# Performance work log

Hardware: AMD Instinct MI355X
Metric: run time of the kernel (lower is better)

The kernel has to match this reference:

```python
import jax, jax.numpy as jnp
import numpy as np

E, HID, T, B, NH, DFF, A, C = 116, 64, 512, 64, 4, 2048, 116, 90


def _ln(x, g, b, eps=1e-5):
    m = x.mean(-1, keepdims=True)
    v = ((x - m) ** 2).mean(-1, keepdims=True)
    return (x - m) / jnp.sqrt(v + eps) * g + b


def _layer(x, p):
    # torch TransformerEncoderLayer, post-norm, relu, eval mode (no dropout)
    wqkv, bqkv, wo, bo, g1, bn1, w1, b1, w2, b2, g2, bn2 = p
    S, N, Em = x.shape  # note: S is the attended axis (dim 0), N the batched axis
    dh = Em // NH
    qkv = x @ wqkv.T + bqkv
    q, k, v = jnp.split(qkv, 3, axis=-1)
    q = q.reshape(S, N, NH, dh)
    k = k.reshape(S, N, NH, dh)
    v = v.reshape(S, N, NH, dh)
    scores = jnp.einsum('snhd,tnhd->nhst', q, k) / np.float32(np.sqrt(dh))
    attn = jax.nn.softmax(scores, axis=-1)
    o = jnp.einsum('nhst,tnhd->snhd', attn, v).reshape(S, N, Em)
    o = o @ wo.T + bo
    x = _ln(x + o, g1, bn1)
    f = jax.nn.relu(x @ w1.T + b1) @ w2.T + b2
    return _ln(x + f, g2, bn2)


def _forward(x, sim, p1, p2, fc_w, fc_b):
    out = _layer(x, p1)
    out1 = _layer(out, p2)
    outs = jnp.transpose(out1, (0, 2, 1))       # (B, E, T)
    fea_ = outs @ fc_w.T + fc_b                 # (B, E, HID)
    feas = jnp.transpose(fea_, (0, 2, 1))       # (B, HID, E)
    fea = feas[:, None, :, :, None]             # (B,1,HID,E,1)
    sim32 = sim.astype(jnp.float32)             # (A, HID, C)
    # cosine_similarity over the HID axis (dim=2 of broadcast tensors),
    # computed without materializing the (B,A,HID,E,C) broadcast product.
    dot = jnp.einsum('bhd,ahc->badc', feas, sim32)           # (B,A,E,C)
    fn = jnp.linalg.norm(feas, axis=1)                       # (B,E)
    sn = jnp.linalg.norm(sim32, axis=1)                      # (A,C)
    denom = jnp.maximum(fn[:, None, :, None] * sn[None, :, None, :], 1e-8)
    similarity = dot / denom                                 # (B,A,E,C)
    similar = similarity.reshape(-1, 116 * 90)
    nrm = jnp.maximum(jnp.linalg.norm(similar, axis=1, keepdims=True), 1e-12)
    similar = similar / nrm
    return fea, similarity, similar


_PNAMES = ['wqkv', 'bqkv', 'wo', 'bo', 'g1', 'bn1', 'w1', 'b1', 'w2', 'b2', 'g2', 'bn2']
_PSHAPES = [(3 * E, E), (3 * E,), (E, E), (E,), (E,), (E,), (DFF, E), (DFF,), (E, DFF), (E,), (E,), (E,)]


def setup_inputs() -> dict:
    key = jax.random.key(0)
    ks = jax.random.split(key, 32)
    s = 0.02
    inp = {
        'x': jax.random.normal(ks[0], (B, T, E), jnp.float32),
        'sim': jax.random.normal(ks[1], (A, HID, C), jnp.float32),
    }
    i = 2
    for L in ('l1', 'l2'):
        for nm, sh in zip(_PNAMES, _PSHAPES):
            if nm in ('g1', 'g2'):
                inp[f'{L}_{nm}'] = jnp.ones(sh, jnp.float32)
            elif nm in ('bqkv', 'bo', 'bn1', 'b1', 'b2', 'bn2'):
                inp[f'{L}_{nm}'] = jnp.zeros(sh, jnp.float32)
            else:
                inp[f'{L}_{nm}'] = jax.random.normal(ks[i], sh, jnp.float32) * s
                i += 1
    inp['fc_w'] = jax.random.normal(ks[i], (HID, T), jnp.float32) * s
    inp['fc_b'] = jnp.zeros((HID,), jnp.float32)
    return inp


def reference(x, sim,
              l1_wqkv, l1_bqkv, l1_wo, l1_bo, l1_g1, l1_bn1, l1_w1, l1_b1, l1_w2, l1_b2, l1_g2, l1_bn2,
              l2_wqkv, l2_bqkv, l2_wo, l2_bo, l2_g1, l2_bn1, l2_w1, l2_b1, l2_w2, l2_b2, l2_g2, l2_bn2,
              fc_w, fc_b):
    p1 = (l1_wqkv, l1_bqkv, l1_wo, l1_bo, l1_g1, l1_bn1, l1_w1, l1_b1, l1_w2, l1_b2, l1_g2, l1_bn2)
    p2 = (l2_wqkv, l2_bqkv, l2_wo, l2_bo, l2_g1, l2_bn1, l2_w1, l2_b1, l2_w2, l2_b2, l2_g2, l2_bn2)
    return _forward(x, sim, p1, p2, fc_w, fc_b)
```

## Files before the change

kernel.cpp:

```cpp
#include <hip/hip_runtime.h>
#include <hip/hip_bf16.h>

typedef __attribute__((ext_vector_type(8))) short short8v;
typedef __attribute__((ext_vector_type(4))) float floatx4;

__device__ __forceinline__ float bf2f(unsigned short u) {
  union { unsigned int i; float f; } c;
  c.i = ((unsigned int)u) << 16;
  return c.f;
}
__device__ __forceinline__ unsigned short f2bf(float f) {
  __hip_bfloat16 h = __float2bfloat16(f);
  return *reinterpret_cast<unsigned short*>(&h);
}

struct ConvJobs {
  const float* src[9];
  unsigned short* dst[9];
  int K[9];
  int Kp[9];
  int mode[9];
  int cum[10];
};

__global__ __launch_bounds__(256) void convert_all_kernel(ConvJobs J) {
  const int total = J.cum[9];
  for (int idx = blockIdx.x * 256 + threadIdx.x; idx < total;
       idx += gridDim.x * 256) {
    int j = 0;
    while (idx >= J.cum[j + 1]) ++j;
    const int local = idx - J.cum[j];
    const int Kp = J.Kp[j];
    const int r = local / Kp, c = local - r * Kp;
    unsigned short v;
    if (J.mode[j] == 0) {
      v = (c < J.K[j]) ? f2bf(J.src[j][(size_t)r * J.K[j] + c])
                       : (unsigned short)0;
    } else {
      const int h = c >> 5, d = c & 31;
      v = (d < 29) ? f2bf(J.src[j][(size_t)r * 116 + h * 29 + d])
                   : (unsigned short)0;
    }
    J.dst[j][local] = v;
  }
}

template <int MODE>
__global__ __launch_bounds__(256) void mgemm_kernel(
    const unsigned short* __restrict__ A, const unsigned short* __restrict__ B,
    const float* __restrict__ bias, int N, int Kp, int ldout,
    unsigned short* __restrict__ Yb) {
  __shared__ __align__(16) unsigned short As[128][64];
  __shared__ __align__(16) unsigned short Bs[128][64];

  const int tid = threadIdx.x;
  const int M0 = blockIdx.x * 128;
  const int N0 = blockIdx.y * 128;
  const int wid = tid >> 6, lane = tid & 63;
  const int wr = wid >> 1, wc = wid & 1;
  const int lc = lane & 15, g = lane >> 4;
  const int srow = tid >> 1, shalf = tid & 1;
  const int sw = srow & 7;

  floatx4 acc[4][4] = {};

  const int nk = Kp >> 6;
  for (int kt = 0; kt < nk; ++kt) {
    const int k0 = kt << 6;
    {
      const uint4* p = reinterpret_cast<const uint4*>(
          A + (size_t)(M0 + srow) * Kp + k0 + shalf * 32);
      uint4 v0 = p[0], v1 = p[1], v2 = p[2], v3 = p[3];
      *reinterpret_cast<uint4*>(&As[srow][((((shalf << 2) | 0) ^ sw) << 3)]) = v0;
      *reinterpret_cast<uint4*>(&As[srow][((((shalf << 2) | 1) ^ sw) << 3)]) = v1;
      *reinterpret_cast<uint4*>(&As[srow][((((shalf << 2) | 2) ^ sw) << 3)]) = v2;
      *reinterpret_cast<uint4*>(&As[srow][((((shalf << 2) | 3) ^ sw) << 3)]) = v3;
    }
    {
      uint4 v0 = {0, 0, 0, 0}, v1 = v0, v2 = v0, v3 = v0;
      const int jr = N0 + srow;
      if (jr < N) {
        const uint4* p = reinterpret_cast<const uint4*>(
            B + (size_t)jr * Kp + k0 + shalf * 32);
        v0 = p[0]; v1 = p[1]; v2 = p[2]; v3 = p[3];
      }
      *reinterpret_cast<uint4*>(&Bs[srow][((((shalf << 2) | 0) ^ sw) << 3)]) = v0;
      *reinterpret_cast<uint4*>(&Bs[srow][((((shalf << 2) | 1) ^ sw) << 3)]) = v1;
      *reinterpret_cast<uint4*>(&Bs[srow][((((shalf << 2) | 2) ^ sw) << 3)]) = v2;
      *reinterpret_cast<uint4*>(&Bs[srow][((((shalf << 2) | 3) ^ sw) << 3)]) = v3;
    }
    __syncthreads();
#pragma unroll
    for (int ks = 0; ks < 2; ++ks) {
      short8v a[4], b[4];
#pragma unroll
      for (int m = 0; m < 4; ++m) {
        const int row = wr * 64 + m * 16 + lc;
        a[m] = *reinterpret_cast<const short8v*>(
            &As[row][((((ks << 2) | g) ^ (lc & 7)) << 3)]);
      }
#pragma unroll
      for (int n = 0; n < 4; ++n) {
        const int col = wc * 64 + n * 16 + lc;
        b[n] = *reinterpret_cast<const short8v*>(
            &Bs[col][((((ks << 2) | g) ^ (lc & 7)) << 3)]);
      }
#pragma unroll
      for (int m = 0; m < 4; ++m)
#pragma unroll
        for (int n = 0; n < 4; ++n)
          acc[m][n] = __builtin_amdgcn_mfma_f32_16x16x32_bf16(a[m], b[n],
                                                              acc[m][n], 0, 0, 0);
    }
    __syncthreads();
  }

#pragma unroll
  for (int m = 0; m < 4; ++m) {
#pragma unroll
    for (int r = 0; r < 4; ++r) {
      const int row = M0 + wr * 64 + m * 16 + g * 4 + r;
#pragma unroll
      for (int n = 0; n < 4; ++n) {
        const int col = N0 + wc * 64 + n * 16 + lc;
        if (col < N) {
          float v = acc[m][n][r] + bias[col];
          if (MODE == 1) v = fmaxf(v, 0.f);
          if constexpr (MODE == 3) {
            const int which = (col >= 232) ? 2 : (col >= 116 ? 1 : 0);
            const int cw = col - which * 116;
            const int h = (cw * 565) >> 14;
            const int d = cw - h * 29;
            const int nn2 = row & 511, ss = row >> 9;
            Yb[(size_t)which * 4194304 +
               ((((size_t)nn2 * 4 + h) * 64 + ss) << 5) + d] = f2bf(v);
          } else {
            Yb[(size_t)row * ldout + col] = f2bf(v);
          }
        }
      }
    }
  }
}

__global__ __launch_bounds__(256) void mgemm64_ln_kernel(
    const unsigned short* __restrict__ A, const unsigned short* __restrict__ B,
    const float* __restrict__ bias, int Kp, unsigned short* __restrict__ Yb,
    float* __restrict__ Yf, const float* __restrict__ res,
    const float* __restrict__ gw, const float* __restrict__ bw) {
  __shared__ __align__(16) unsigned short As[64][64];
  __shared__ __align__(16) unsigned short Bs[128][64];
  __shared__ float sum1[2][64];
  __shared__ float sum2[2][64];

  const int tid = threadIdx.x;
  const int M0 = blockIdx.x * 64;
  const int wid = tid >> 6, lane = tid & 63;
  const int wr = wid >> 1, wc = wid & 1;
  const int lc = lane & 15, g = lane >> 4;
  const int arow = tid >> 2, aq = tid & 3;
  const int brow = tid >> 1, bhalf = tid & 1;

  floatx4 acc[2][4] = {};

  const int nk = Kp >> 6;
  for (int kt = 0; kt < nk; ++kt) {
    const int k0 = kt << 6;
    {
      const uint4* p = reinterpret_cast<const uint4*>(
          A + (size_t)(M0 + arow) * Kp + k0 + aq * 16);
      uint4 v0 = p[0], v1 = p[1];
      const int swa = arow & 7;
      *reinterpret_cast<uint4*>(&As[arow][(((aq * 2) ^ swa) << 3)]) = v0;
      *reinterpret_cast<uint4*>(&As[arow][(((aq * 2 + 1) ^ swa) << 3)]) = v1;
    }
    {
      uint4 v0 = {0, 0, 0, 0}, v1 = v0, v2 = v0, v3 = v0;
      if (brow < 116) {
        const uint4* p = reinterpret_cast<const uint4*>(
            B + (size_t)brow * Kp + k0 + bhalf * 32);
        v0 = p[0]; v1 = p[1]; v2 = p[2]; v3 = p[3];
      }
      const int sw = brow & 7;
      *reinterpret_cast<uint4*>(&Bs[brow][((((bhalf << 2) | 0) ^ sw) << 3)]) = v0;
      *reinterpret_cast<uint4*>(&Bs[brow][((((bhalf << 2) | 1) ^ sw) << 3)]) = v1;
      *reinterpret_cast<uint4*>(&Bs[brow][((((bhalf << 2) | 2) ^ sw) << 3)]) = v2;
      *reinterpret_cast<uint4*>(&Bs[brow][((((bhalf << 2) | 3) ^ sw) << 3)]) = v3;
    }
    __syncthreads();
#pragma unroll
    for (int ks = 0; ks < 2; ++ks) {
      short8v a[2], b[4];
#pragma unroll
      for (int m = 0; m < 2; ++m) {
        const int row = wr * 32 + m * 16 + lc;
        a[m] = *reinterpret_cast<const short8v*>(
            &As[row][((((ks << 2) | g) ^ (row & 7)) << 3)]);
      }
#pragma unroll
      for (int n = 0; n < 4; ++n) {
        const int col = wc * 64 + n * 16 + lc;
        b[n] = *reinterpret_cast<const short8v*>(
            &Bs[col][((((ks << 2) | g) ^ (col & 7)) << 3)]);
      }
#pragma unroll
      for (int m = 0; m < 2; ++m)
#pragma unroll
        for (int n = 0; n < 4; ++n)
          acc[m][n] = __builtin_amdgcn_mfma_f32_16x16x32_bf16(a[m], b[n],
                                                              acc[m][n], 0, 0, 0);
    }
    __syncthreads();
  }

  float s1l[2][4], s2l[2][4];
#pragma unroll
  for (int m = 0; m < 2; ++m) {
#pragma unroll
    for (int r = 0; r < 4; ++r) {
      const int row = M0 + wr * 32 + m * 16 + g * 4 + r;
      float s = 0.f, s2 = 0.f;
#pragma unroll
      for (int n = 0; n < 4; ++n) {
        const int col = wc * 64 + n * 16 + lc;
        float v = 0.f;
        if (col < 116)
          v = acc[m][n][r] + bias[col] + res[(size_t)row * 116 + col];
        acc[m][n][r] = v;
        s += v;
        s2 = fmaf(v, v, s2);
      }
#pragma unroll
      for (int st = 1; st < 16; st <<= 1) {
        s += __shfl_xor(s, st, 16);
        s2 += __shfl_xor(s2, st, 16);
      }
      s1l[m][r] = s;
      s2l[m][r] = s2;
    }
  }
  if (lc == 0) {
#pragma unroll
    for (int m = 0; m < 2; ++m)
#pragma unroll
      for (int r = 0; r < 4; ++r) {
        const int lrow = wr * 32 + m * 16 + g * 4 + r;
        sum1[wc][lrow] = s1l[m][r];
        sum2[wc][lrow] = s2l[m][r];
      }
  }
  __syncthreads();
#pragma unroll
  for (int m = 0; m < 2; ++m) {
#pragma unroll
    for (int r = 0; r < 4; ++r) {
      const int lrow = wr * 32 + m * 16 + g * 4 + r;
      const int row = M0 + lrow;
      const float st = sum1[0][lrow] + sum1[1][lrow];
      const float s2t = sum2[0][lrow] + sum2[1][lrow];
      const float mean = st * (1.f / 116.f);
      const float var = s2t * (1.f / 116.f) - mean * mean;
      const float rstd = 1.f / sqrtf(var + 1e-5f);
#pragma unroll
      for (int n = 0; n < 4; ++n) {
        const int col = wc * 64 + n * 16 + lc;
        if (col < 116) {
          const float y = (acc[m][n][r] - mean) * rstd * gw[col] + bw[col];
          Yf[(size_t)row * 116 + col] = y;
          Yb[(size_t)row * 128 + col] = f2bf(y);
        } else {
          Yb[(size_t)row * 128 + col] = 0;
        }
      }
    }
  }
}

__global__ __launch_bounds__(256) void ffn_fused_kernel(
    const unsigned short* __restrict__ Xa,
    const unsigned short* __restrict__ W1,
    const float* __restrict__ b1,
    const unsigned short* __restrict__ W2,
    const float* __restrict__ b2, const float* __restrict__ res,
    const float* __restrict__ gw, const float* __restrict__ bw,
    unsigned short* __restrict__ Yb,
    float* __restrict__ Yf) {
  __shared__ __align__(16) unsigned short Xs[64][128];
  __shared__ __align__(16) unsigned short W1c[64][128];
  __shared__ __align__(16) unsigned short W2c[128][64];
  __shared__ __align__(16) unsigned short Hs[64][64];
  __shared__ float sum1[2][64];
  __shared__ float sum2[2][64];

  const int tid = threadIdx.x;
  const int M0 = blockIdx.x * 64;
  const int wid = tid >> 6, lane = tid & 63;
  const int wr = wid >> 1, wc = wid & 1;
  const int lc = lane & 15, g = lane >> 4;
  const int arow = tid >> 2, aq = tid & 3;
  const int brow = tid >> 1, bh = tid & 1;

  {
    const uint4* p = reinterpret_cast<const uint4*>(
        Xa + (size_t)(M0 + arow) * 128 + aq * 32);
#pragma unroll
    for (int q = 0; q < 4; ++q) {
      const int cj = aq * 4 + q;
      const int swz = (cj & 8) | ((cj ^ arow) & 7);
      *reinterpret_cast<uint4*>(&Xs[arow][swz * 8]) = p[q];
    }
  }

  uint4 w1r[4], w2r[4];
  {
    const uint4* p1 =
        reinterpret_cast<const uint4*>(W1 + (size_t)arow * 128 + aq * 32);
#pragma unroll
    for (int q = 0; q < 4; ++q) w1r[q] = p1[q];
    uint4 z = {0, 0, 0, 0};
    w2r[0] = z; w2r[1] = z; w2r[2] = z; w2r[3] = z;
    if (brow < 116) {
      const uint4* p2 =
          reinterpret_cast<const uint4*>(W2 + (size_t)brow * 2048 + bh * 32);
#pragma unroll
      for (int q = 0; q < 4; ++q) w2r[q] = p2[q];
    }
  }

  floatx4 oacc[2][4] = {};

  for (int kc = 0; kc < 32; ++kc) {
#pragma unroll
    for (int q = 0; q < 4; ++q) {
      const int cj = aq * 4 + q;
      const int swz = (cj & 8) | ((cj ^ arow) & 7);
      *reinterpret_cast<uint4*>(&W1c[arow][swz * 8]) = w1r[q];
    }
#pragma unroll
    for (int q = 0; q < 4; ++q) {
      const int cj = bh * 4 + q;
      const int swz = (cj ^ brow) & 7;
      *reinterpret_cast<uint4*>(&W2c[brow][swz * 8]) = w2r[q];
    }
    if (kc < 31) {
      const uint4* p1 = reinterpret_cast<const uint4*>(
          W1 + (size_t)((kc + 1) * 64 + arow) * 128 + aq * 32);
#pragma unroll
      for (int q = 0; q < 4; ++q) w1r[q] = p1[q];
      if (brow < 116) {
        const uint4* p2 = reinterpret_cast<const uint4*>(
            W2 + (size_t)brow * 2048 + (kc + 1) * 64 + bh * 32);
#pragma unroll
        for (int q = 0; q < 4; ++q) w2r[q] = p2[q];
      }
    }
    __syncthreads();

    floatx4 hacc[2][2] = {};
#pragma unroll
    for (int ks = 0; ks < 4; ++ks) {
      short8v av[2], bv[2];
#pragma unroll
      for (int m = 0; m < 2; ++m) {
        const int row = wr * 32 + m * 16 + lc;
        const int cj = ks * 4 + g;
        const int swz = (cj & 8) | ((cj ^ row) & 7);
        av[m] = *reinterpret_cast<const short8v*>(&Xs[row][swz * 8]);
      }
#pragma unroll
      for (int n = 0; n < 2; ++n) {
        const int row = wc * 32 + n * 16 + lc;
        const int cj = ks * 4 + g;
        const int swz = (cj & 8) | ((cj ^ row) & 7);
        bv[n] = *reinterpret_cast<const short8v*>(&W1c[row][swz * 8]);
      }
#pragma unroll
      for (int m = 0; m < 2; ++m)
#pragma unroll
        for (int n = 0; n < 2; ++n)
          hacc[m][n] = __builtin_amdgcn_mfma_f32_16x16x32_bf16(av[m], bv[n],
                                                               hacc[m][n], 0, 0, 0);
    }
#pragma unroll
    for (int n = 0; n < 2; ++n) {
      const int dff = wc * 32 + n * 16 + lc;
      const float bb = b1[kc * 64 + dff];
      const int cj = dff >> 3;
      const int dlo = dff & 7;
#pragma unroll
      for (int m = 0; m < 2; ++m) {
#pragma unroll
        for (int r = 0; r < 4; ++r) {
          const int tok = wr * 32 + m * 16 + g * 4 + r;
          const float hv = fmaxf(hacc[m][n][r] + bb, 0.f);
          Hs[tok][(((cj ^ tok) & 7) << 3) | dlo] = f2bf(hv);
        }
      }
    }
    __syncthreads();

#pragma unroll
    for (int ks = 0; ks < 2; ++ks) {
      short8v av[2], bv[4];
#pragma unroll
      for (int m = 0; m < 2; ++m) {
        const int row = wr * 32 + m * 16 + lc;
        const int cj = ks * 4 + g;
        av[m] = *reinterpret_cast<const short8v*>(
            &Hs[row][(((cj ^ row) & 7) << 3)]);
      }
#pragma unroll
      for (int n = 0; n < 4; ++n) {
        const int col = wc * 64 + n * 16 + lc;
        const int cj = ks * 4 + g;
        bv[n] = *reinterpret_cast<const short8v*>(
            &W2c[col][(((cj ^ col) & 7) << 3)]);
      }
#pragma unroll
      for (int m = 0; m < 2; ++m)
#pragma unroll
        for (int n = 0; n < 4; ++n)
          oacc[m][n] = __builtin_amdgcn_mfma_f32_16x16x32_bf16(av[m], bv[n],
                                                               oacc[m][n], 0, 0, 0);
    }
    __syncthreads();
  }

  float s1l[2][4], s2l[2][4];
#pragma unroll
  for (int m = 0; m < 2; ++m) {
#pragma unroll
    for (int r = 0; r < 4; ++r) {
      const int row = M0 + wr * 32 + m * 16 + g * 4 + r;
      float s = 0.f, s2 = 0.f;
#pragma unroll
      for (int n = 0; n < 4; ++n) {
        const int col = wc * 64 + n * 16 + lc;
        float v = 0.f;
        if (col < 116)
          v = oacc[m][n][r] + b2[col] + res[(size_t)row * 116 + col];
        oacc[m][n][r] = v;
        s += v;
        s2 = fmaf(v, v, s2);
      }
#pragma unroll
      for (int st = 1; st < 16; st <<= 1) {
        s += __shfl_xor(s, st, 16);
        s2 += __shfl_xor(s2, st, 16);
      }
      s1l[m][r] = s;
      s2l[m][r] = s2;
    }
  }
  if (lc == 0) {
#pragma unroll
    for (int m = 0; m < 2; ++m)
#pragma unroll
      for (int r = 0; r < 4; ++r) {
        const int lrow = wr * 32 + m * 16 + g * 4 + r;
        sum1[wc][lrow] = s1l[m][r];
        sum2[wc][lrow] = s2l[m][r];
      }
  }
  __syncthreads();
#pragma unroll
  for (int m = 0; m < 2; ++m) {
#pragma unroll
    for (int r = 0; r < 4; ++r) {
      const int lrow = wr * 32 + m * 16 + g * 4 + r;
      const int row = M0 + lrow;
      const float st = sum1[0][lrow] + sum1[1][lrow];
      const float s2t = sum2[0][lrow] + sum2[1][lrow];
      const float mean = st * (1.f / 116.f);
      const float var = s2t * (1.f / 116.f) - mean * mean;
      const float rstd = 1.f / sqrtf(var + 1e-5f);
#pragma unroll
      for (int n = 0; n < 4; ++n) {
        const int col = wc * 64 + n * 16 + lc;
        if (col < 116) {
          const float y = (oacc[m][n][r] - mean) * rstd * gw[col] + bw[col];
          Yf[(size_t)row * 116 + col] = y;
          Yb[(size_t)row * 128 + col] = f2bf(y);
        } else {
          Yb[(size_t)row * 128 + col] = 0;
        }
      }
    }
  }
}

__global__ __launch_bounds__(64) void attn_kernel(
    const unsigned short* __restrict__ qkvp, unsigned short* __restrict__ obuf) {
  const int h = blockIdx.x & 3;
  const int n = blockIdx.x >> 2;
  const int s = threadIdx.x;
  __shared__ float ks[64][36];
  __shared__ float vs[64][36];

  const size_t rb = (((size_t)n * 4 + h) * 64 + s) * 32;
  const uint4* qp = reinterpret_cast<const uint4*>(qkvp + rb);
  const uint4* kp = reinterpret_cast<const uint4*>(qkvp + 4194304 + rb);
  const uint4* vp = reinterpret_cast<const uint4*>(qkvp + 8388608 + rb);
  uint4 qv[4], kv4[4], vv4[4];
#pragma unroll
  for (int i = 0; i < 4; ++i) {
    qv[i] = qp[i];
    kv4[i] = kp[i];
    vv4[i] = vp[i];
  }
  float q[32], kf[32], vf[32];
#pragma unroll
  for (int i = 0; i < 4; ++i) {
    const unsigned* wq = reinterpret_cast<const unsigned*>(&qv[i]);
    const unsigned* wk = reinterpret_cast<const unsigned*>(&kv4[i]);
    const unsigned* wv = reinterpret_cast<const unsigned*>(&vv4[i]);
#pragma unroll
    for (int j = 0; j < 4; ++j) {
      union { unsigned u; float f; } lo, hi;
      const int d0 = i * 8 + 2 * j;
      lo.u = wq[j] << 16; hi.u = wq[j] & 0xffff0000u;
      q[d0] = lo.f; q[d0 + 1] = hi.f;
      lo.u = wk[j] << 16; hi.u = wk[j] & 0xffff0000u;
      kf[d0] = (d0 < 29) ? lo.f : 0.f;
      kf[d0 + 1] = (d0 + 1 < 29) ? hi.f : 0.f;
      lo.u = wv[j] << 16; hi.u = wv[j] & 0xffff0000u;
      vf[d0] = (d0 < 29) ? lo.f : 0.f;
      vf[d0 + 1] = (d0 + 1 < 29) ? hi.f : 0.f;
    }
  }
  q[29] = q[30] = q[31] = 0.f;
#pragma unroll
  for (int c = 0; c < 8; ++c) {
    *reinterpret_cast<float4*>(&ks[s][c * 4]) =
        make_float4(kf[4 * c], kf[4 * c + 1], kf[4 * c + 2], kf[4 * c + 3]);
    *reinterpret_cast<float4*>(&vs[s][c * 4]) =
        make_float4(vf[4 * c], vf[4 * c + 1], vf[4 * c + 2], vf[4 * c + 3]);
  }
  __syncthreads();

  const float scale = 0.18569533817705186f;
  float sc[64];
#pragma unroll 4
  for (int t = 0; t < 64; ++t) {
    const float4* kr = reinterpret_cast<const float4*>(&ks[t][0]);
    float a = 0.f;
#pragma unroll
    for (int c = 0; c < 8; ++c) {
      const float4 kc = kr[c];
      a = fmaf(q[4 * c], kc.x, a);
      a = fmaf(q[4 * c + 1], kc.y, a);
      a = fmaf(q[4 * c + 2], kc.z, a);
      a = fmaf(q[4 * c + 3], kc.w, a);
    }
    sc[t] = a * scale;
  }
  float m = sc[0];
#pragma unroll
  for (int t = 1; t < 64; ++t) m = fmaxf(m, sc[t]);
  float sum = 0.f;
#pragma unroll
  for (int t = 0; t < 64; ++t) {
    sc[t] = __expf(sc[t] - m);
    sum += sc[t];
  }
  const float inv = 1.f / sum;
  float o[32] = {};
#pragma unroll 4
  for (int t = 0; t < 64; ++t) {
    const float p = sc[t];
    const float4* vr = reinterpret_cast<const float4*>(&vs[t][0]);
#pragma unroll
    for (int c = 0; c < 8; ++c) {
      const float4 vc = vr[c];
      o[4 * c] = fmaf(p, vc.x, o[4 * c]);
      o[4 * c + 1] = fmaf(p, vc.y, o[4 * c + 1]);
      o[4 * c + 2] = fmaf(p, vc.z, o[4 * c + 2]);
      o[4 * c + 3] = fmaf(p, vc.w, o[4 * c + 3]);
    }
  }
  unsigned short ow[32];
#pragma unroll
  for (int i = 0; i < 32; ++i) ow[i] = f2bf(o[i] * inv);
  uint4* od =
      reinterpret_cast<uint4*>(obuf + ((size_t)s * 512 + n) * 128 + h * 32);
  const uint4* ows = reinterpret_cast<const uint4*>(ow);
#pragma unroll
  for (int i = 0; i < 4; ++i) od[i] = ows[i];
}

__global__ __launch_bounds__(256) void fc_kernel(
    const float* __restrict__ X4, const float* __restrict__ fw,
    const float* __restrict__ fb, float* __restrict__ fea,
    unsigned short* __restrict__ feaT, float* __restrict__ fn) {
  const int eg = blockIdx.x;
  const int b = blockIdx.y;
  const int e0 = eg * 29;
  __shared__ float Os[64][30];
  __shared__ float Wf[64][65];
  const int tid = threadIdx.x;
  const int h = tid & 63, jg = tid >> 6;
  float acc[8] = {};

  for (int tc = 0; tc < 8; ++tc) {
    for (int idx = tid; idx < 64 * 29; idx += 256) {
      int tt = idx / 29;
      int ee = idx - tt * 29;
      Os[tt][ee] = X4[((size_t)b * 512 + tc * 64 + tt) * 116 + e0 + ee];
    }
    for (int idx = tid; idx < 64 * 64; idx += 256) {
      int hh = idx >> 6, t2 = idx & 63;
      Wf[hh][t2] = fw[(size_t)hh * 512 + tc * 64 + t2];
    }
    __syncthreads();
#pragma unroll 4
    for (int t = 0; t < 64; ++t) {
      const float w = Wf[h][t];
#pragma unroll
      for (int m = 0; m < 8; ++m) {
        const int el = jg + 4 * m;
        if (el < 29) acc[m] = fmaf(Os[t][el], w, acc[m]);
      }
    }
    __syncthreads();
  }
  const float bb = fb[h];
#pragma unroll
  for (int m = 0; m < 8; ++m) {
    const int el = jg + 4 * m;
    if (el < 29) {
      const float v = acc[m] + bb;
      const int e = e0 + el;
      fea[((size_t)b * 64 + h) * 116 + e] = v;
      if (feaT) {
        const unsigned short vb = f2bf(v);
        feaT[((size_t)b * 128 + e) * 64 + h] = vb;
        float s = bf2f(vb);
        s = s * s;
#pragma unroll
        for (int st = 1; st <= 32; st <<= 1) s += __shfl_xor(s, st, 64);
        if (h == 0) fn[b * 128 + e] = sqrtf(s);
      }
    }
  }
}

__global__ __launch_bounds__(256) void simt_prep_kernel(
    const float* __restrict__ simin, unsigned short* __restrict__ simT,
    float* __restrict__ sn) {
  __shared__ float L[64][91];
  const int a = blockIdx.x;
  const int tid = threadIdx.x;
  for (int idx = tid; idx < 64 * 90; idx += 256) {
    const int h = idx / 90, c = idx - h * 90;
    L[h][c] = bf2f(f2bf(simin[((size_t)a * 64 + h) * 90 + c]));
  }
  __syncthreads();
  for (int idx = tid; idx < 96 * 64; idx += 256) {
    const int c = idx >> 6, h = idx & 63;
    simT[((size_t)a * 96 + c) * 64 + h] = (c < 90) ? f2bf(L[h][c]) : 0;
  }
  if (tid < 90) {
    float s = 0.f;
#pragma unroll 8
    for (int h = 0; h < 64; ++h) {
      const float t = L[h][tid];
      s = fmaf(t, t, s);
    }
    sn[a * 96 + tid] = sqrtf(s);
  }
}

__global__ __launch_bounds__(256) void sim_mfma3_kernel(
    const unsigned short* __restrict__ feaT, const unsigned short* __restrict__ simT,
    const float* __restrict__ fn, const float* __restrict__ sn,
    float* __restrict__ simil, float* __restrict__ similar) {
  const int a0 = blockIdx.x * 4;
  const int b = blockIdx.y;
  __shared__ __align__(16) unsigned short Ft[128][64];
  __shared__ __align__(16) unsigned short St[96][64];
  __shared__ __align__(16) float Rs[10440];
  __shared__ float fnrow[116];
  __shared__ float snrow[90];
  __shared__ float wred[4];
  const int tid = threadIdx.x;
  const int srow = tid >> 1, shalf = tid & 1;
  const int sw = srow & 7;
  const int wid = tid >> 6, lane = tid & 63;
  const int wr = wid >> 1, wc = wid & 1;
  const int lc = lane & 15, g = lane >> 4;

  {
    const uint4* p = reinterpret_cast<const uint4*>(
        feaT + ((size_t)b * 128 + srow) * 64 + shalf * 32);
    uint4 v0 = p[0], v1 = p[1], v2 = p[2], v3 = p[3];
    *reinterpret_cast<uint4*>(&Ft[srow][((((shalf << 2) | 0) ^ sw) << 3)]) = v0;
    *reinterpret_cast<uint4*>(&Ft[srow][((((shalf << 2) | 1) ^ sw) << 3)]) = v1;
    *reinterpret_cast<uint4*>(&Ft[srow][((((shalf << 2) | 2) ^ sw) << 3)]) = v2;
    *reinterpret_cast<uint4*>(&Ft[srow][((((shalf << 2) | 3) ^ sw) << 3)]) = v3;
  }
  if (tid < 116) fnrow[tid] = fn[b * 128 + tid];

  for (int ai = 0; ai < 4; ++ai) {
    const int a = a0 + ai;
    if (srow < 96) {
      const uint4* p = reinterpret_cast<const uint4*>(
          simT + ((size_t)a * 96 + srow) * 64 + shalf * 32);
      uint4 v0 = p[0], v1 = p[1], v2 = p[2], v3 = p[3];
      *reinterpret_cast<uint4*>(&St[srow][((((shalf << 2) | 0) ^ sw) << 3)]) = v0;
      *reinterpret_cast<uint4*>(&St[srow][((((shalf << 2) | 1) ^ sw) << 3)]) = v1;
      *reinterpret_cast<uint4*>(&St[srow][((((shalf << 2) | 2) ^ sw) << 3)]) = v2;
      *reinterpret_cast<uint4*>(&St[srow][((((shalf << 2) | 3) ^ sw) << 3)]) = v3;
    }
    if (tid >= 160 && tid < 250) snrow[tid - 160] = sn[a * 96 + (tid - 160)];
    __syncthreads();

    floatx4 acc[4][3] = {};
#pragma unroll
    for (int ks = 0; ks < 2; ++ks) {
      short8v av[4], bv[3];
#pragma unroll
      for (int m = 0; m < 4; ++m) {
        const int row = wr * 64 + m * 16 + lc;
        av[m] = *reinterpret_cast<const short8v*>(
            &Ft[row][((((ks << 2) | g) ^ (lc & 7)) << 3)]);
      }
#pragma unroll
      for (int n = 0; n < 3; ++n) {
        const int col = wc * 48 + n * 16 + lc;
        bv[n] = *reinterpret_cast<const short8v*>(
            &St[col][((((ks << 2) | g) ^ (lc & 7)) << 3)]);
      }
#pragma unroll
      for (int m = 0; m < 4; ++m)
#pragma unroll
        for (int n = 0; n < 3; ++n)
          acc[m][n] = __builtin_amdgcn_mfma_f32_16x16x32_bf16(av[m], bv[n],
                                                              acc[m][n], 0, 0, 0);
    }

    float ss = 0.f;
#pragma unroll
    for (int m = 0; m < 4; ++m) {
#pragma unroll
      for (int r = 0; r < 4; ++r) {
        const int d = wr * 64 + m * 16 + g * 4 + r;
        if (d < 116) {
          const float fnv = fnrow[d];
#pragma unroll
          for (int n = 0; n < 3; ++n) {
            const int c = wc * 48 + n * 16 + lc;
            if (c < 90) {
              const float denom = fmaxf(fnv * snrow[c], 1e-8f);
              float rcp = __builtin_amdgcn_rcpf(denom);
              rcp = rcp * (2.0f - denom * rcp);
              const float v = acc[m][n][r] * rcp;
              ss = fmaf(v, v, ss);
              Rs[d * 90 + c] = v;
            }
          }
        }
      }
    }
#pragma unroll
    for (int st = 1; st <= 32; st <<= 1) ss += __shfl_xor(ss, st, 64);
    if (lane == 0) wred[wid] = ss;
    __syncthreads();
    const float tot = wred[0] + wred[1] + wred[2] + wred[3];
    const float inv = 1.f / fmaxf(sqrtf(tot), 1e-12f);

    const size_t rowbase = ((size_t)b * 116 + a) * (116 * 90);
    float4* so = reinterpret_cast<float4*>(simil + rowbase);
    float4* sr = reinterpret_cast<float4*>(similar + rowbase);
    const float4* rs4 = reinterpret_cast<const float4*>(Rs);
    for (int i = tid; i < 2610; i += 256) {
      float4 v = rs4[i];
      so[i] = v;
      float4 w;
      w.x = v.x * inv; w.y = v.y * inv; w.z = v.z * inv; w.w = v.w * inv;
      sr[i] = w;
    }
  }
}

__global__ __launch_bounds__(256) void sim_mfma_kernel(
    const float* __restrict__ fea, const float* __restrict__ simin,
    float* __restrict__ simil, float* __restrict__ similar) {
  const int a = blockIdx.x;
  const int b = blockIdx.y;
  __shared__ __align__(16) unsigned char shmem[41760];
  __shared__ float fnrow[116];
  __shared__ float snrow[90];
  __shared__ float wred[4];
  const int tid = threadIdx.x;

  unsigned short (*Ft)[64] = reinterpret_cast<unsigned short(*)[64]>(shmem);
  unsigned short (*St)[64] =
      reinterpret_cast<unsigned short(*)[64]>(shmem + 16384);
  float* Rs = reinterpret_cast<float*>(shmem);

  for (int idx = tid; idx < 64 * 116; idx += 256) {
    const int h = idx / 116, d = idx - h * 116;
    Ft[d][(((h >> 3) ^ (d & 7)) << 3) | (h & 7)] =
        f2bf(fea[((size_t)b * 64 + h) * 116 + d]);
  }
  for (int idx = tid; idx < 12 * 64; idx += 256) {
    const int d = 116 + (idx >> 6), h = idx & 63;
    Ft[d][(((h >> 3) ^ (d & 7)) << 3) | (h & 7)] = 0;
  }
  for (int idx = tid; idx < 64 * 90; idx += 256) {
    const int h = idx / 90, c = idx - h * 90;
    St[c][(((h >> 3) ^ (c & 7)) << 3) | (h & 7)] =
        f2bf(simin[((size_t)a * 64 + h) * 90 + c]);
  }
  for (int idx = tid; idx < 6 * 64; idx += 256) {
    const int c = 90 + (idx >> 6), h = idx & 63;
    St[c][(((h >> 3) ^ (c & 7)) << 3) | (h & 7)] = 0;
  }
  __syncthreads();

  if (tid < 116) {
    float s = 0.f;
#pragma unroll 8
    for (int h = 0; h < 64; ++h) {
      const float t = bf2f(Ft[tid][(((h >> 3) ^ (tid & 7)) << 3) | (h & 7)]);
      s = fmaf(t, t, s);
    }
    fnrow[tid] = sqrtf(s);
  } else if (tid >= 128 && tid < 218) {
    const int c = tid - 128;
    float s = 0.f;
#pragma unroll 8
    for (int h = 0; h < 64; ++h) {
      const float t = bf2f(St[c][(((h >> 3) ^ (c & 7)) << 3) | (h & 7)]);
      s = fmaf(t, t, s);
    }
    snrow[c] = sqrtf(s);
  }
  __syncthreads();

  const int wid = tid >> 6, lane = tid & 63;
  const int wr = wid >> 1, wc = wid & 1;
  const int lc = lane & 15, g = lane >> 4;

  floatx4 acc[4][3] = {};
#pragma unroll
  for (int ks = 0; ks < 2; ++ks) {
    short8v av[4], bv[3];
#pragma unroll
    for (int m = 0; m < 4; ++m) {
      const int row = wr * 64 + m * 16 + lc;
      av[m] = *reinterpret_cast<const short8v*>(
          &Ft[row][((((ks << 2) | g) ^ (lc & 7)) << 3)]);
    }
#pragma unroll
    for (int n = 0; n < 3; ++n) {
      const int col = wc * 48 + n * 16 + lc;
      bv[n] = *reinterpret_cast<const short8v*>(
          &St[col][((((ks << 2) | g) ^ (lc & 7)) << 3)]);
    }
#pragma unroll
    for (int m = 0; m < 4; ++m)
#pragma unroll
      for (int n = 0; n < 3; ++n)
        acc[m][n] = __builtin_amdgcn_mfma_f32_16x16x32_bf16(av[m], bv[n],
                                                            acc[m][n], 0, 0, 0);
  }
  __syncthreads();

  float ss = 0.f;
#pragma unroll
  for (int m = 0; m < 4; ++m) {
#pragma unroll
    for (int r = 0; r < 4; ++r) {
      const int d = wr * 64 + m * 16 + g * 4 + r;
      if (d < 116) {
        const float fnv = fnrow[d];
#pragma unroll
        for (int n = 0; n < 3; ++n) {
          const int c = wc * 48 + n * 16 + lc;
          if (c < 90) {
            const float denom = fmaxf(fnv * snrow[c], 1e-8f);
            float rcp = __builtin_amdgcn_rcpf(denom);
            rcp = rcp * (2.0f - denom * rcp);
            const float v = acc[m][n][r] * rcp;
            ss = fmaf(v, v, ss);
            Rs[d * 90 + c] = v;
          }
        }
      }
    }
  }
#pragma unroll
  for (int st = 1; st <= 32; st <<= 1) ss += __shfl_xor(ss, st, 64);
  if (lane == 0) wred[wid] = ss;
  __syncthreads();
  const float tot = wred[0] + wred[1] + wred[2] + wred[3];
  const float inv = 1.f / fmaxf(sqrtf(tot), 1e-12f);

  const size_t rowbase = ((size_t)b * 116 + a) * (116 * 90);
  float4* so = reinterpret_cast<float4*>(simil + rowbase);
  float4* sr = reinterpret_cast<float4*>(similar + rowbase);
  const float4* rs4 = reinterpret_cast<const float4*>(Rs);
  for (int i = tid; i < 2610; i += 256) {
    float4 v = rs4[i];
    so[i] = v;
    float4 w;
    w.x = v.x * inv; w.y = v.y * inv; w.z = v.z * inv; w.w = v.w * inv;
    sr[i] = w;
  }
}

extern "C" void kernel_launch(void* const* d_in, const int* in_sizes, int n_in,
                              void* d_out, int out_size, void* d_ws,
                              size_t ws_size, hipStream_t stream) {
  const float* x0 = (const float*)d_in[0];
  const float* simin = (const float*)d_in[1];
  const float* p[24];
  for (int i = 0; i < 24; ++i) p[i] = (const float*)d_in[2 + i];
  const float* fc_w = (const float*)d_in[26];
  const float* fc_b = (const float*)d_in[27];

  float* out = (float*)d_out;
  float* fea = out;
  float* simil = out + 475136;
  float* similar = out + 77981696;

  float* xa_f[2] = {similar + 0, similar + 7602176};
  float* xb_f[2] = {similar + 3801088, similar + 11403264};
  unsigned short* obufb = (unsigned short*)(similar + 15204352);
  unsigned short* qkvp = (unsigned short*)(similar + 17301504);
  unsigned short* Ab = (unsigned short*)(similar + 23592960);
  unsigned short* xab[2] = {(unsigned short*)(similar + 25690112),
                            (unsigned short*)(similar + 29884416)};
  unsigned short* xbb[2] = {(unsigned short*)(similar + 27787264),
                            (unsigned short*)(similar + 31981568)};
  unsigned short* wbuf = (unsigned short*)(simil + 33554432);
  const size_t WSZ = 559104;

  unsigned char* ws = (unsigned char*)d_ws;
  unsigned short* feaT = (unsigned short*)ws;
  unsigned short* simT = (unsigned short*)(ws + 1048576);
  float* fnb = (float*)(ws + 2473984);
  float* snb = (float*)(ws + 2506752);
  const bool ws_ok = ws_size >= 2551296;

  {
    ConvJobs J;
    int cum = 0;
    auto add = [&](int j, const float* s, unsigned short* dd, int R, int K,
                   int Kp, int mode) {
      J.src[j] = s; J.dst[j] = dd; J.K[j] = K; J.Kp[j] = Kp; J.mode[j] = mode;
      J.cum[j] = cum; cum += R * Kp;
    };
    add(0, x0, Ab, 32768, 116, 128, 0);
    for (int L = 0; L < 2; ++L) {
      unsigned short* wb = wbuf + L * WSZ;
      add(1 + L * 4, p[L * 12 + 0], wb + 0, 348, 116, 128, 0);
      add(2 + L * 4, p[L * 12 + 2], wb + 44544, 116, 116, 128, 1);
      add(3 + L * 4, p[L * 12 + 6], wb + 59392, 2048, 116, 128, 0);
      add(4 + L * 4, p[L * 12 + 8], wb + 321536, 116, 2048, 2048, 0);
    }
    J.cum[9] = cum;
    hipLaunchKernelGGL(convert_all_kernel, dim3(2048), dim3(256), 0, stream, J);
  }

  if (ws_ok) {
    hipLaunchKernelGGL(simt_prep_kernel, dim3(116), dim3(256), 0, stream,
                       simin, simT, snb);
  }

  const unsigned short* Ain = Ab;
  const float* resin = x0;
  for (int L = 0; L < 2; ++L) {
    unsigned short* wb = wbuf + L * WSZ;
    const float* bqkv = p[L * 12 + 1];
    const float* bo = p[L * 12 + 3];
    const float* g1 = p[L * 12 + 4];
    const float* bn1 = p[L * 12 + 5];
    const float* b1 = p[L * 12 + 7];
    const float* b2 = p[L * 12 + 9];
    const float* g2 = p[L * 12 + 10];
    const float* bn2 = p[L * 12 + 11];

    hipLaunchKernelGGL((mgemm_kernel<3>), dim3(256, 3), dim3(256), 0, stream,
                       Ain, wb + 0, bqkv, 348, 128, 0, qkvp);
    hipLaunchKernelGGL(attn_kernel, dim3(2048), dim3(64), 0, stream, qkvp,
                       obufb);
    hipLaunchKernelGGL(mgemm64_ln_kernel, dim3(512), dim3(256), 0, stream,
                       obufb, wb + 44544, bo, 128, xab[L], xa_f[L], resin, g1,
                       bn1);
    hipLaunchKernelGGL(ffn_fused_kernel, dim3(512), dim3(256), 0, stream,
                       xab[L], wb + 59392, b1, wb + 321536, b2, xa_f[L], g2,
                       bn2, xbb[L], xb_f[L]);
    Ain = xbb[L];
    resin = xb_f[L];
  }

  if (ws_ok) {
    hipLaunchKernelGGL(fc_kernel, dim3(4, 64), dim3(256), 0, stream, xb_f[1],
                       fc_w, fc_b, fea, feaT, fnb);
    hipLaunchKernelGGL(sim_mfma3_kernel, dim3(29, 64), dim3(256), 0, stream,
                       feaT, simT, fnb, snb, simil, similar);
  } else {
    hipLaunchKernelGGL(fc_kernel, dim3(4, 64), dim3(256), 0, stream, xb_f[1],
                       fc_w, fc_b, fea, (unsigned short*)nullptr,
                       (float*)nullptr);
    hipLaunchKernelGGL(sim_mfma_kernel, dim3(116, 64), dim3(256), 0, stream,
                       fea, simin, simil, similar);
  }
}
```

Measured before the change: 664.5 us.

## Warp-specialize similarity kernel to overlap MFMA compute with output stores

The similarity kernel now runs 512 threads split into two roles. The first 256 compute the MFMA tile for one anchor and prefetch the next anchor's sim tile into a double buffer. The second 256 normalize and write the previous anchor's results to global memory. This is meant to hide the large store traffic (two float outputs of about 41 KB per anchor) behind compute, in exchange for roughly double the LDS footprint and lower occupancy (launch_bounds 512,1).

After: 675.1 us. Within noise of the previous version (+1.6%).

```diff
diff --git a/kernel.cpp b/kernel.cpp
--- a/kernel.cpp
+++ b/kernel.cpp
@@ -277,14 +277,11 @@
 }
 
 __global__ __launch_bounds__(256) void ffn_fused_kernel(
-    const unsigned short* __restrict__ Xa,
-    const unsigned short* __restrict__ W1,
-    const float* __restrict__ b1,
-    const unsigned short* __restrict__ W2,
+    const unsigned short* __restrict__ Xa, const unsigned short* __restrict__ W1,
+    const float* __restrict__ b1, const unsigned short* __restrict__ W2,
     const float* __restrict__ b2, const float* __restrict__ res,
     const float* __restrict__ gw, const float* __restrict__ bw,
-    unsigned short* __restrict__ Yb,
-    float* __restrict__ Yf) {
+    unsigned short* __restrict__ Yb, float* __restrict__ Yf) {
   __shared__ __align__(16) unsigned short Xs[64][128];
   __shared__ __align__(16) unsigned short W1c[64][128];
   __shared__ __align__(16) unsigned short W2c[128][64];
@@ -670,115 +667,136 @@
   }
 }
 
-__global__ __launch_bounds__(256) void sim_mfma3_kernel(
+__global__ __launch_bounds__(512, 1) void sim_mfma4_kernel(
     const unsigned short* __restrict__ feaT, const unsigned short* __restrict__ simT,
     const float* __restrict__ fn, const float* __restrict__ sn,
     float* __restrict__ simil, float* __restrict__ similar) {
   const int a0 = blockIdx.x * 4;
   const int b = blockIdx.y;
   __shared__ __align__(16) unsigned short Ft[128][64];
-  __shared__ __align__(16) unsigned short St[96][64];
-  __shared__ __align__(16) float Rs[10440];
+  __shared__ __align__(16) unsigned short St[2][96][64];
+  __shared__ __align__(16) float Rs[2][10440];
   __shared__ float fnrow[116];
-  __shared__ float snrow[90];
-  __shared__ float wred[4];
+  __shared__ float snrow[2][90];
+  __shared__ float wred[2][4];
   const int tid = threadIdx.x;
-  const int srow = tid >> 1, shalf = tid & 1;
-  const int sw = srow & 7;
   const int wid = tid >> 6, lane = tid & 63;
-  const int wr = wid >> 1, wc = wid & 1;
-  const int lc = lane & 15, g = lane >> 4;
 
   {
+    const int row = tid >> 2, q4 = tid & 3;
+    const int sw = row & 7;
     const uint4* p = reinterpret_cast<const uint4*>(
-        feaT + ((size_t)b * 128 + srow) * 64 + shalf * 32);
-    uint4 v0 = p[0], v1 = p[1], v2 = p[2], v3 = p[3];
-    *reinterpret_cast<uint4*>(&Ft[srow][((((shalf << 2) | 0) ^ sw) << 3)]) = v0;
-    *reinterpret_cast<uint4*>(&Ft[srow][((((shalf << 2) | 1) ^ sw) << 3)]) = v1;
-    *reinterpret_cast<uint4*>(&Ft[srow][((((shalf << 2) | 2) ^ sw) << 3)]) = v2;
-    *reinterpret_cast<uint4*>(&Ft[srow][((((shalf << 2) | 3) ^ sw) << 3)]) = v3;
+        feaT + ((size_t)b * 128 + row) * 64 + q4 * 16);
+    uint4 v0 = p[0], v1 = p[1];
+    *reinterpret_cast<uint4*>(&Ft[row][(((q4 * 2) ^ sw) << 3)]) = v0;
+    *reinterpret_cast<uint4*>(&Ft[row][(((q4 * 2 + 1) ^ sw) << 3)]) = v1;
   }
   if (tid < 116) fnrow[tid] = fn[b * 128 + tid];
-
-  for (int ai = 0; ai < 4; ++ai) {
-    const int a = a0 + ai;
+  if (tid >= 256) {
+    const int st = tid - 256;
+    const int srow = st >> 1, shalf = st & 1;
     if (srow < 96) {
+      const int sw = srow & 7;
       const uint4* p = reinterpret_cast<const uint4*>(
-          simT + ((size_t)a * 96 + srow) * 64 + shalf * 32);
+          simT + ((size_t)a0 * 96 + srow) * 64 + shalf * 32);
       uint4 v0 = p[0], v1 = p[1], v2 = p[2], v3 = p[3];
-      *reinterpret_cast<uint4*>(&St[srow][((((shalf << 2) | 0) ^ sw) << 3)]) = v0;
-      *reinterpret_cast<uint4*>(&St[srow][((((shalf << 2) | 1) ^ sw) << 3)]) = v1;
-      *reinterpret_cast<uint4*>(&St[srow][((((shalf << 2) | 2) ^ sw) << 3)]) = v2;
-      *reinterpret_cast<uint4*>(&St[srow][((((shalf << 2) | 3) ^ sw) << 3)]) = v3;
-    }
-    if (tid >= 160 && tid < 250) snrow[tid - 160] = sn[a * 96 + (tid - 160)];
-    __syncthreads();
-
-    floatx4 acc[4][3] = {};
-#pragma unroll
-    for (int ks = 0; ks < 2; ++ks) {
-      short8v av[4], bv[3];
+      *reinterpret_cast<uint4*>(&St[0][srow][((((shalf << 2) | 0) ^ sw) << 3)]) = v0;
+      *reinterpret_cast<uint4*>(&St[0][srow][((((shalf << 2) | 1) ^ sw) << 3)]) = v1;
+      *reinterpret_cast<uint4*>(&St[0][srow][((((shalf << 2) | 2) ^ sw) << 3)]) = v2;
+      *reinterpret_cast<uint4*>(&St[0][srow][((((shalf << 2) | 3) ^ sw) << 3)]) = v3;
+    }
+    if (st < 90) snrow[0][st] = sn[a0 * 96 + st];
+  }
+  __syncthreads();
+
+  for (int ai = 0; ai < 5; ++ai) {
+    if (tid < 256 && ai < 4) {
+      const int cb = ai & 1;
+      const int wr = wid >> 1, wc = wid & 1;
+      const int lc = lane & 15, g = lane >> 4;
+      floatx4 acc[4][3] = {};
+#pragma unroll
+      for (int ks = 0; ks < 2; ++ks) {
+        short8v av[4], bv[3];
+#pragma unroll
+        for (int m = 0; m < 4; ++m) {
+          const int row = wr * 64 + m * 16 + lc;
+          av[m] = *reinterpret_cast<const short8v*>(
+              &Ft[row][((((ks << 2) | g) ^ (lc & 7)) << 3)]);
+        }
+#pragma unroll
+        for (int n = 0; n < 3; ++n) {
+          const int col = wc * 48 + n * 16 + lc;
+          bv[n] = *reinterpret_cast<const short8v*>(
+              &St[cb][col][((((ks << 2) | g) ^ (lc & 7)) << 3)]);
+        }
+#pragma unroll
+        for (int m = 0; m < 4; ++m)
+#pragma unroll
+          for (int n = 0; n < 3; ++n)
+            acc[m][n] = __builtin_amdgcn_mfma_f32_16x16x32_bf16(
+                av[m], bv[n], acc[m][n], 0, 0, 0);
+      }
+      float ss = 0.f;
 #pragma unroll
       for (int m = 0; m < 4; ++m) {
-        const int row = wr * 64 + m * 16 + lc;
-        av[m] = *reinterpret_cast<const short8v*>(
-            &Ft[row][((((ks << 2) | g) ^ (lc & 7)) << 3)]);
-      }
-#pragma unroll
-      for (int n = 0; n < 3; ++n) {
-        const int col = wc * 48 + n * 16 + lc;
-        bv[n] = *reinterpret_cast<const short8v*>(
-            &St[col][((((ks << 2) | g) ^ (lc & 7)) << 3)]);
-      }
-#pragma unroll
-      for (int m = 0; m < 4; ++m)
-#pragma unroll
-        for (int n = 0; n < 3; ++n)
-          acc[m][n] = __builtin_amdgcn_mfma_f32_16x16x32_bf16(av[m], bv[n],
-                                                              acc[m][n], 0, 0, 0);
-    }
-
-    float ss = 0.f;
-#pragma unroll
-    for (int m = 0; m < 4; ++m) {
-#pragma unroll
-      for (int r = 0; r < 4; ++r) {
-        const int d = wr * 64 + m * 16 + g * 4 + r;
-        if (d < 116) {
-          const float fnv = fnrow[d];
-#pragma unroll
-          for (int n = 0; n < 3; ++n) {
-            const int c = wc * 48 + n * 16 + lc;
-            if (c < 90) {
-              const float denom = fmaxf(fnv * snrow[c], 1e-8f);
-              float rcp = __builtin_amdgcn_rcpf(denom);
-              rcp = rcp * (2.0f - denom * rcp);
-              const float v = acc[m][n][r] * rcp;
-              ss = fmaf(v, v, ss);
-              Rs[d * 90 + c] = v;
+#pragma unroll
+        for (int r = 0; r < 4; ++r) {
+          const int d = wr * 64 + m * 16 + g * 4 + r;
+          if (d < 116) {
+            const float fnv = fnrow[d];
+#pragma unroll
+            for (int n = 0; n < 3; ++n) {
+              const int c = wc * 48 + n * 16 + lc;
+              if (c < 90) {
+                const float denom = fmaxf(fnv * snrow[cb][c], 1e-8f);
+                float rcp = __builtin_amdgcn_rcpf(denom);
+                rcp = rcp * (2.0f - denom * rcp);
+                const float v = acc[m][n][r] * rcp;
+                ss = fmaf(v, v, ss);
+                Rs[cb][d * 90 + c] = v;
+              }
             }
           }
         }
       }
-    }
-#pragma unroll
-    for (int st = 1; st <= 32; st <<= 1) ss += __shfl_xor(ss, st, 64);
-    if (lane == 0) wred[wid] = ss;
+#pragma unroll
+      for (int st = 1; st <= 32; st <<= 1) ss += __shfl_xor(ss, st, 64);
+      if (lane == 0) wred[cb][wid] = ss;
+      if (ai < 3) {
+        const int nb = cb ^ 1;
+        const int anext = a0 + ai + 1;
+        const int srow = tid >> 1, shalf = tid & 1;
+        if (srow < 96) {
+          const int sw = srow & 7;
+          const uint4* p = reinterpret_cast<const uint4*>(
+              simT + ((size_t)anext * 96 + srow) * 64 + shalf * 32);
+          uint4 v0 = p[0], v1 = p[1], v2 = p[2], v3 = p[3];
+          *reinterpret_cast<uint4*>(&St[nb][srow][((((shalf << 2) | 0) ^ sw) << 3)]) = v0;
+          *reinterpret_cast<uint4*>(&St[nb][srow][((((shalf << 2) | 1) ^ sw) << 3)]) = v1;
+          *reinterpret_cast<uint4*>(&St[nb][srow][((((shalf << 2) | 2) ^ sw) << 3)]) = v2;
+          *reinterpret_cast<uint4*>(&St[nb][srow][((((shalf << 2) | 3) ^ sw) << 3)]) = v3;
+        }
+        if (tid >= 160 && tid < 250) snrow[nb][tid - 160] = sn[anext * 96 + tid - 160];
+      }
+    } else if (tid >= 256 && ai >= 1) {
+      const int pb = (ai - 1) & 1;
+      const float tot = wred[pb][0] + wred[pb][1] + wred[pb][2] + wred[pb][3];
+      const float inv = 1.f / fmaxf(sqrtf(tot), 1e-12f);
+      const int a = a0 + ai - 1;
+      const size_t rowbase = ((size_t)b * 116 + a) * (116 * 90);
+      float4* so = reinterpret_cast<float4*>(simil + rowbase);
+      float4* sr = reinterpret_cast<float4*>(similar + rowbase);
+      const float4* rs4 = reinterpret_cast<const float4*>(Rs[pb]);
+      for (int i = tid - 256; i < 2610; i += 256) {
+        float4 v = rs4[i];
+        so[i] = v;
+        float4 w;
+        w.x = v.x * inv; w.y = v.y * inv; w.z = v.z * inv; w.w = v.w * inv;
+        sr[i] = w;
+      }
+    }
     __syncthreads();
-    const float tot = wred[0] + wred[1] + wred[2] + wred[3];
-    const float inv = 1.f / fmaxf(sqrtf(tot), 1e-12f);
-
-    const size_t rowbase = ((size_t)b * 116 + a) * (116 * 90);
-    float4* so = reinterpret_cast<float4*>(simil + rowbase);
-    float4* sr = reinterpret_cast<float4*>(similar + rowbase);
-    const float4* rs4 = reinterpret_cast<const float4*>(Rs);
-    for (int i = tid; i < 2610; i += 256) {
-      float4 v = rs4[i];
-      so[i] = v;
-      float4 w;
-      w.x = v.x * inv; w.y = v.y * inv; w.z = v.z * inv; w.w = v.w * inv;
-      sr[i] = w;
-    }
   }
 }
 
@@ -999,7 +1017,7 @@
   if (ws_ok) {
     hipLaunchKernelGGL(fc_kernel, dim3(4, 64), dim3(256), 0, stream, xb_f[1],
                        fc_w, fc_b, fea, feaT, fnb);
-    hipLaunchKernelGGL(sim_mfma3_kernel, dim3(29, 64), dim3(256), 0, stream,
+    hipLaunchKernelGGL(sim_mfma4_kernel, dim3(29, 64), dim3(512), 0, stream,
                        feaT, simT, fnb, snb, simil, similar);
   } else {
     hipLaunchKernelGGL(fc_kernel, dim3(4, 64), dim3(256), 0, stream, xb_f[1],
```

## Enlarge fused FFN tiles to 128 tokens and 128-wide DFF chunks

Applied to the files above, without the earlier changes.

The fused FFN kernel now runs 512-thread blocks over 128-token tiles and walks the 2048-wide hidden dimension in 128-wide chunks instead of 64. Each weight chunk loaded into shared memory is reused across twice as many tokens, which halves total weight traffic and halves the number of K-loop iterations and barriers. The hidden-activation buffer switches from XOR swizzling to a padded row stride of 136. The trade-off is a larger shared-memory footprint, occupancy limited to one block per CU, and only 256 blocks, which may leave some CUs underused.

Measured after the change: 620.7 us. -6.6%, faster.

```diff
diff --git a/kernel.cpp b/kernel.cpp
--- a/kernel.cpp
+++ b/kernel.cpp
@@ -276,7 +276,7 @@
   }
 }
 
-__global__ __launch_bounds__(256) void ffn_fused_kernel(
+__global__ __launch_bounds__(512, 1) void ffn_fused2_kernel(
     const unsigned short* __restrict__ Xa,
     const unsigned short* __restrict__ W1,
     const float* __restrict__ b1,
@@ -285,43 +285,42 @@
     const float* __restrict__ gw, const float* __restrict__ bw,
     unsigned short* __restrict__ Yb,
     float* __restrict__ Yf) {
-  __shared__ __align__(16) unsigned short Xs[64][128];
-  __shared__ __align__(16) unsigned short W1c[64][128];
-  __shared__ __align__(16) unsigned short W2c[128][64];
-  __shared__ __align__(16) unsigned short Hs[64][64];
-  __shared__ float sum1[2][64];
-  __shared__ float sum2[2][64];
+  __shared__ __align__(16) unsigned short Xs[128][128];
+  __shared__ __align__(16) unsigned short W1c[128][128];
+  __shared__ __align__(16) unsigned short W2c[128][128];
+  __shared__ __align__(16) unsigned short Hs[128][136];
+  __shared__ float sum1[2][128];
+  __shared__ float sum2[2][128];
 
   const int tid = threadIdx.x;
-  const int M0 = blockIdx.x * 64;
+  const int M0 = blockIdx.x * 128;
   const int wid = tid >> 6, lane = tid & 63;
-  const int wr = wid >> 1, wc = wid & 1;
+  const int wtr = wid >> 1, wdc = wid & 1;
   const int lc = lane & 15, g = lane >> 4;
-  const int arow = tid >> 2, aq = tid & 3;
-  const int brow = tid >> 1, bh = tid & 1;
+  const int srow = tid >> 2, aq = tid & 3;
 
   {
     const uint4* p = reinterpret_cast<const uint4*>(
-        Xa + (size_t)(M0 + arow) * 128 + aq * 32);
+        Xa + (size_t)(M0 + srow) * 128 + aq * 32);
 #pragma unroll
     for (int q = 0; q < 4; ++q) {
       const int cj = aq * 4 + q;
-      const int swz = (cj & 8) | ((cj ^ arow) & 7);
-      *reinterpret_cast<uint4*>(&Xs[arow][swz * 8]) = p[q];
+      const int swz = (cj & 8) | ((cj ^ srow) & 7);
+      *reinterpret_cast<uint4*>(&Xs[srow][swz * 8]) = p[q];
     }
   }
 
   uint4 w1r[4], w2r[4];
   {
     const uint4* p1 =
-        reinterpret_cast<const uint4*>(W1 + (size_t)arow * 128 + aq * 32);
+        reinterpret_cast<const uint4*>(W1 + (size_t)srow * 128 + aq * 32);
 #pragma unroll
     for (int q = 0; q < 4; ++q) w1r[q] = p1[q];
     uint4 z = {0, 0, 0, 0};
     w2r[0] = z; w2r[1] = z; w2r[2] = z; w2r[3] = z;
-    if (brow < 116) {
+    if (srow < 116) {
       const uint4* p2 =
-          reinterpret_cast<const uint4*>(W2 + (size_t)brow * 2048 + bh * 32);
+          reinterpret_cast<const uint4*>(W2 + (size_t)srow * 2048 + aq * 32);
 #pragma unroll
       for (int q = 0; q < 4; ++q) w2r[q] = p2[q];
     }
@@ -329,92 +328,81 @@
 
   floatx4 oacc[2][4] = {};
 
-  for (int kc = 0; kc < 32; ++kc) {
+  for (int kc = 0; kc < 16; ++kc) {
 #pragma unroll
     for (int q = 0; q < 4; ++q) {
       const int cj = aq * 4 + q;
-      const int swz = (cj & 8) | ((cj ^ arow) & 7);
-      *reinterpret_cast<uint4*>(&W1c[arow][swz * 8]) = w1r[q];
-    }
-#pragma unroll
-    for (int q = 0; q < 4; ++q) {
-      const int cj = bh * 4 + q;
-      const int swz = (cj ^ brow) & 7;
-      *reinterpret_cast<uint4*>(&W2c[brow][swz * 8]) = w2r[q];
-    }
-    if (kc < 31) {
+      const int swz = (cj & 8) | ((cj ^ srow) & 7);
+      *reinterpret_cast<uint4*>(&W1c[srow][swz * 8]) = w1r[q];
+      *reinterpret_cast<uint4*>(&W2c[srow][swz * 8]) = w2r[q];
+    }
+    if (kc < 15) {
       const uint4* p1 = reinterpret_cast<const uint4*>(
-          W1 + (size_t)((kc + 1) * 64 + arow) * 128 + aq * 32);
+          W1 + (size_t)((kc + 1) * 128 + srow) * 128 + aq * 32);
 #pragma unroll
       for (int q = 0; q < 4; ++q) w1r[q] = p1[q];
-      if (brow < 116) {
+      if (srow < 116) {
         const uint4* p2 = reinterpret_cast<const uint4*>(
-            W2 + (size_t)brow * 2048 + (kc + 1) * 64 + bh * 32);
+            W2 + (size_t)srow * 2048 + (kc + 1) * 128 + aq * 32);
 #pragma unroll
         for (int q = 0; q < 4; ++q) w2r[q] = p2[q];
       }
     }
     __syncthreads();
 
-    floatx4 hacc[2][2] = {};
+    floatx4 hacc[2][4] = {};
 #pragma unroll
     for (int ks = 0; ks < 4; ++ks) {
-      short8v av[2], bv[2];
+      short8v av[2], bv[4];
+      const int cj = ks * 4 + g;
 #pragma unroll
       for (int m = 0; m < 2; ++m) {
-        const int row = wr * 32 + m * 16 + lc;
-        const int cj = ks * 4 + g;
+        const int row = wtr * 32 + m * 16 + lc;
         const int swz = (cj & 8) | ((cj ^ row) & 7);
         av[m] = *reinterpret_cast<const short8v*>(&Xs[row][swz * 8]);
       }
 #pragma unroll
-      for (int n = 0; n < 2; ++n) {
-        const int row = wc * 32 + n * 16 + lc;
-        const int cj = ks * 4 + g;
+      for (int n = 0; n < 4; ++n) {
+        const int row = wdc * 64 + n * 16 + lc;
         const int swz = (cj & 8) | ((cj ^ row) & 7);
         bv[n] = *reinterpret_cast<const short8v*>(&W1c[row][swz * 8]);
       }
 #pragma unroll
       for (int m = 0; m < 2; ++m)
 #pragma unroll
-        for (int n = 0; n < 2; ++n)
+        for (int n = 0; n < 4; ++n)
           hacc[m][n] = __builtin_amdgcn_mfma_f32_16x16x32_bf16(av[m], bv[n],
                                                                hacc[m][n], 0, 0, 0);
     }
 #pragma unroll
-    for (int n = 0; n < 2; ++n) {
-      const int dff = wc * 32 + n * 16 + lc;
-      const float bb = b1[kc * 64 + dff];
-      const int cj = dff >> 3;
-      const int dlo = dff & 7;
+    for (int n = 0; n < 4; ++n) {
+      const int dff = wdc * 64 + n * 16 + lc;
+      const float bb = b1[kc * 128 + dff];
 #pragma unroll
       for (int m = 0; m < 2; ++m) {
 #pragma unroll
         for (int r = 0; r < 4; ++r) {
-          const int tok = wr * 32 + m * 16 + g * 4 + r;
-          const float hv = fmaxf(hacc[m][n][r] + bb, 0.f);
-          Hs[tok][(((cj ^ tok) & 7) << 3) | dlo] = f2bf(hv);
+          const int tok = wtr * 32 + m * 16 + g * 4 + r;
+          Hs[tok][dff] = f2bf(fmaxf(hacc[m][n][r] + bb, 0.f));
         }
       }
     }
     __syncthreads();
 
 #pragma unroll
-    for (int ks = 0; ks < 2; ++ks) {
+    for (int ks = 0; ks < 4; ++ks) {
       short8v av[2], bv[4];
+      const int cj = ks * 4 + g;
 #pragma unroll
       for (int m = 0; m < 2; ++m) {
-        const int row = wr * 32 + m * 16 + lc;
-        const int cj = ks * 4 + g;
-        av[m] = *reinterpret_cast<const short8v*>(
-            &Hs[row][(((cj ^ row) & 7) << 3)]);
+        const int row = wtr * 32 + m * 16 + lc;
+        av[m] = *reinterpret_cast<const short8v*>(&Hs[row][cj * 8]);
       }
 #pragma unroll
       for (int n = 0; n < 4; ++n) {
-        const int col = wc * 64 + n * 16 + lc;
-        const int cj = ks * 4 + g;
-        bv[n] = *reinterpret_cast<const short8v*>(
-            &W2c[col][(((cj ^ col) & 7) << 3)]);
+        const int col = wdc * 64 + n * 16 + lc;
+        const int swz = (cj & 8) | ((cj ^ col) & 7);
+        bv[n] = *reinterpret_cast<const short8v*>(&W2c[col][swz * 8]);
       }
 #pragma unroll
       for (int m = 0; m < 2; ++m)
@@ -431,11 +419,11 @@
   for (int m = 0; m < 2; ++m) {
 #pragma unroll
     for (int r = 0; r < 4; ++r) {
-      const int row = M0 + wr * 32 + m * 16 + g * 4 + r;
+      const int row = M0 + wtr * 32 + m * 16 + g * 4 + r;
       float s = 0.f, s2 = 0.f;
 #pragma unroll
       for (int n = 0; n < 4; ++n) {
-        const int col = wc * 64 + n * 16 + lc;
+        const int col = wdc * 64 + n * 16 + lc;
         float v = 0.f;
         if (col < 116)
           v = oacc[m][n][r] + b2[col] + res[(size_t)row * 116 + col];
@@ -457,9 +445,9 @@
     for (int m = 0; m < 2; ++m)
 #pragma unroll
       for (int r = 0; r < 4; ++r) {
-        const int lrow = wr * 32 + m * 16 + g * 4 + r;
-        sum1[wc][lrow] = s1l[m][r];
-        sum2[wc][lrow] = s2l[m][r];
+        const int lrow = wtr * 32 + m * 16 + g * 4 + r;
+        sum1[wdc][lrow] = s1l[m][r];
+        sum2[wdc][lrow] = s2l[m][r];
       }
   }
   __syncthreads();
@@ -467,7 +455,7 @@
   for (int m = 0; m < 2; ++m) {
 #pragma unroll
     for (int r = 0; r < 4; ++r) {
-      const int lrow = wr * 32 + m * 16 + g * 4 + r;
+      const int lrow = wtr * 32 + m * 16 + g * 4 + r;
       const int row = M0 + lrow;
       const float st = sum1[0][lrow] + sum1[1][lrow];
       const float s2t = sum2[0][lrow] + sum2[1][lrow];
@@ -476,7 +464,7 @@
       const float rstd = 1.f / sqrtf(var + 1e-5f);
 #pragma unroll
       for (int n = 0; n < 4; ++n) {
-        const int col = wc * 64 + n * 16 + lc;
+        const int col = wdc * 64 + n * 16 + lc;
         if (col < 116) {
           const float y = (oacc[m][n][r] - mean) * rstd * gw[col] + bw[col];
           Yf[(size_t)row * 116 + col] = y;
@@ -989,7 +977,7 @@
     hipLaunchKernelGGL(mgemm64_ln_kernel, dim3(512), dim3(256), 0, stream,
                        obufb, wb + 44544, bo, 128, xab[L], xa_f[L], resin, g1,
                        bn1);
-    hipLaunchKernelGGL(ffn_fused_kernel, dim3(512), dim3(256), 0, stream,
+    hipLaunchKernelGGL(ffn_fused2_kernel, dim3(256), dim3(512), 0, stream,
                        xab[L], wb + 59392, b1, wb + 321536, b2, xa_f[L], g2,
                        bn2, xbb[L], xb_f[L]);
     Ain = xbb[L];
```
